# Kernel tuning notes

Measured on AMD Instinct MI355X. Metric: run time of the kernel, lower is better.

Reference implementation:

```python
import jax, jax.numpy as jnp
import numpy as np

NUM_CODES = 100000
NUM_EDGES = 20000
DIM = 128
DEG = 32  # nodes per hyperedge -> 640000 incidences


def setup_inputs() -> dict:
    key = jax.random.key(0)
    k1, k2, k3, k4, k5 = jax.random.split(key, 5)
    n_inc = NUM_EDGES * DEG
    # incidence list: edge_ids is sorted (CSR-style), node_ids are member nodes
    node_ids = jax.random.randint(k1, (n_inc,), 0, NUM_CODES, dtype=jnp.int32)
    edge_ids = jnp.repeat(jnp.arange(NUM_EDGES, dtype=jnp.int32), DEG)
    # learned parameters (xavier-ish scales)
    node_emb = jax.random.normal(k2, (NUM_CODES, DIM), jnp.float32) * (1.0 / np.sqrt(DIM))
    edge_emb = jax.random.normal(k3, (NUM_EDGES, DIM), jnp.float32) * (1.0 / np.sqrt(DIM))
    W_e = jax.random.normal(k4, (DIM, DIM), jnp.float32) * (1.0 / np.sqrt(DIM))
    b_e = jnp.zeros((DIM,), jnp.float32)
    W_v = jax.random.normal(k5, (DIM, DIM), jnp.float32) * (1.0 / np.sqrt(DIM))
    b_v = jnp.zeros((DIM,), jnp.float32)
    return {"node_emb": node_emb, "edge_emb": edge_emb, "W_e": W_e, "b_e": b_e,
            "W_v": W_v, "b_v": b_v, "node_ids": node_ids, "edge_ids": edge_ids}


def reference(node_emb, edge_emb, W_e, b_e, W_v, b_v, node_ids, edge_ids):
    N, D = node_emb.shape
    E = edge_emb.shape[0]
    # node -> edge: mean of member node embeddings per hyperedge (segment mean)
    gathered = node_emb[node_ids]                                    # [I, D]
    seg_sum = jax.ops.segment_sum(gathered, edge_ids, num_segments=E)  # [E, D]
    seg_cnt = jax.ops.segment_sum(jnp.ones_like(edge_ids, jnp.float32), edge_ids, num_segments=E)
    mean = seg_sum / jnp.maximum(seg_cnt, 1.0)[:, None]
    # empty edges fall back to their own edge embedding (as in the torch loop)
    edge_ctx = jnp.where(seg_cnt[:, None] > 0, mean, edge_emb)
    edge_ctx = edge_ctx @ W_e.T + b_e                                # lin_e
    # edge -> node: scatter-add edge_ctx back to member nodes
    node_sum = jnp.zeros_like(node_emb).at[node_ids].add(edge_ctx[edge_ids])
    deg = jnp.zeros((N,), jnp.float32).at[node_ids].add(1.0)
    node_cnt = 1.0 + deg  # torch code clamps zeros to 1 BEFORE adding counts
    node_ctx = (node_sum / node_cnt[:, None]) @ W_v.T + b_v          # lin_v
    node_out = node_emb + node_ctx
    edge_out = edge_emb + edge_ctx
    return (node_out, edge_out)
```

## Files before the change

### kernel.cpp

```cpp
#include <hip/hip_runtime.h>

#define DIMS 128
#define DEG 32
#define CAP 32

typedef __attribute__((ext_vector_type(8))) short short8;
typedef __attribute__((ext_vector_type(4))) float floatx4;

static __device__ __forceinline__ unsigned short f2bf(float f) {
  unsigned int u = __float_as_uint(f);
  unsigned int r = (u + 0x7FFFu + ((u >> 16) & 1u)) >> 16;
  return (unsigned short)r;
}
static __device__ __forceinline__ float bf2f(unsigned short v) {
  return __uint_as_float(((unsigned int)v) << 16);
}

__global__ __launch_bounds__(256) void k_prep(
    const float* __restrict__ node_emb, unsigned short* __restrict__ nb, int n0,
    const float* __restrict__ We_f, unsigned short* __restrict__ web, int n1,
    const float* __restrict__ Wv, const float* __restrict__ be,
    unsigned short* __restrict__ Wc, float* __restrict__ bc,
    int* __restrict__ cnt, int ncnt,
    unsigned short* __restrict__ zrow) {
  int b = blockIdx.x;
  int tid = threadIdx.x;
  if (b < 16) {
    __shared__ __align__(16) float wv_s[8][DIMS];
    int d0 = b * 8;
    {
      int row = tid >> 5, c4 = tid & 31;
      *(float4*)&wv_s[row][c4 * 4] = ((const float4*)(Wv + (size_t)d0 * DIMS))[tid];
    }
    __syncthreads();
    int dd = tid >> 5;
    int k4 = (tid & 31) * 4;
    float4 acc = {0.f, 0.f, 0.f, 0.f};
    for (int c = 0; c < DIMS; ++c) {
      float w = wv_s[dd][c];
      float4 we = *(const float4*)(We_f + (size_t)c * DIMS + k4);
      acc.x += w * we.x; acc.y += w * we.y; acc.z += w * we.z; acc.w += w * we.w;
    }
    ushort4 o;
    o.x = f2bf(acc.x); o.y = f2bf(acc.y); o.z = f2bf(acc.z); o.w = f2bf(acc.w);
    *(ushort4*)(Wc + (size_t)(d0 + dd) * DIMS + k4) = o;
    return;
  }
  if (b == 16) {
    __shared__ float be_s[DIMS];
    if (tid < DIMS) be_s[tid] = be[tid];
    if (tid >= 128 && tid < 144) {
      short8 z = {0, 0, 0, 0, 0, 0, 0, 0};
      *(short8*)(zrow + (size_t)(tid - 128) * 8) = z;
    }
    __syncthreads();
    if (tid < DIMS) {
      float s = 0.f;
      for (int c = 0; c < DIMS; ++c) s += Wv[(size_t)tid * DIMS + c] * be_s[c];
      bc[tid] = s;
    }
    return;
  }
  int base = (b - 17) * 256 + tid;
  int stride = (gridDim.x - 17) * 256;
  for (int t = base; t < ncnt; t += stride) cnt[t] = 0;
  int n4 = (n0 + n1) >> 2;
  for (int i4 = base; i4 < n4; i4 += stride) {
    int i = i4 * 4;
    const float* s; unsigned short* d;
    if (i < n0) { s = node_emb + i; d = nb + i; }
    else { s = We_f + (i - n0); d = web + (i - n0); }
    float4 v = *(const float4*)s;
    ushort4 o;
    o.x = f2bf(v.x); o.y = f2bf(v.y); o.z = f2bf(v.z); o.w = f2bf(v.w);
    *(ushort4*)d = o;
  }
}

__global__ __launch_bounds__(256) void k_edge_fused(
    const unsigned short* __restrict__ node_emb_bf,
    const int* __restrict__ node_ids,
    const unsigned short* __restrict__ We,
    const unsigned short* __restrict__ Wc,
    const float* __restrict__ be,
    const float* __restrict__ bc,
    const float* __restrict__ edge_emb,
    float* __restrict__ edge_out,
    unsigned short* __restrict__ ectx2,
    int* __restrict__ cnt,
    unsigned short* __restrict__ bucket,
    int E) {
  int e0 = blockIdx.x * 16;
  int tid = threadIdx.x;
  __shared__ int ids[16][DEG];
  __shared__ __align__(16) unsigned short xs[16 * DIMS];
#pragma unroll
  for (int u = 0; u < 2; ++u) {
    int idx = tid + u * 256;
    int ee = idx >> 5, j = idx & 31;
    int e = e0 + ee;
    ids[ee][j] = (e < E) ? node_ids[(size_t)e * DEG + j] : 0;
  }
  __syncthreads();

  {
    int ee = tid >> 4;
    int l8 = tid & 15;
    float acc[8] = {0.f, 0.f, 0.f, 0.f, 0.f, 0.f, 0.f, 0.f};
#pragma unroll
    for (int jb = 0; jb < DEG; jb += 8) {
      short8 v[8];
#pragma unroll
      for (int u = 0; u < 8; ++u) {
        int n = ids[ee][jb + u];
        v[u] = *(const short8*)(node_emb_bf + (size_t)n * DIMS + l8 * 8);
      }
#pragma unroll
      for (int u = 0; u < 8; ++u)
#pragma unroll
        for (int t = 0; t < 8; ++t) acc[t] += bf2f((unsigned short)v[u][t]);
    }
    const float s = 1.0f / (float)DEG;
    short8 o;
#pragma unroll
    for (int t = 0; t < 8; ++t) o[t] = (short)f2bf(acc[t] * s);
    int byt = ee * 256 + ((l8 * 16) ^ ((ee & 7) << 4));
    *(short8*)((char*)xs + byt) = o;
  }

  {
    int ia = tid, ib = tid + 256;
    int ea = e0 + (ia >> 5), eb = e0 + (ib >> 5);
    int na = ids[ia >> 5][ia & 31];
    int nb_ = ids[ib >> 5][ib & 31];
    int pa = CAP, pb = CAP;
    bool va = ea < E, vb = eb < E;
    if (va) pa = atomicAdd(&cnt[na], 1);
    if (vb) pb = atomicAdd(&cnt[nb_], 1);
    if (va && pa < CAP) bucket[(size_t)na * CAP + pa] = (unsigned short)ea;
    if (vb && pb < CAP) bucket[(size_t)nb_ * CAP + pb] = (unsigned short)eb;
  }
  __syncthreads();

  int wave = tid >> 6;
  int lane = tid & 63;
  int ln = lane & 15;
  int quad = lane >> 4;

  floatx4 acc_e0 = {0.f,0.f,0.f,0.f}, acc_e1 = {0.f,0.f,0.f,0.f};
  floatx4 acc_c0 = {0.f,0.f,0.f,0.f}, acc_c1 = {0.f,0.f,0.f,0.f};

#pragma unroll
  for (int kc = 0; kc < 4; ++kc) {
    int bofs = ln * 256 + ((kc * 64 + quad * 16) ^ ((ln & 7) << 4));
    short8 a = *(const short8*)((const char*)xs + bofs);
    int kb = kc * 32 + quad * 8;
    int wr0 = wave * 32 + ln;
    int wr1 = wave * 32 + 16 + ln;
    short8 bwe0 = *(const short8*)(We + (size_t)wr0 * DIMS + kb);
    short8 bwc0 = *(const short8*)(Wc + (size_t)wr0 * DIMS + kb);
    short8 bwe1 = *(const short8*)(We + (size_t)wr1 * DIMS + kb);
    short8 bwc1 = *(const short8*)(Wc + (size_t)wr1 * DIMS + kb);
    acc_e0 = __builtin_amdgcn_mfma_f32_16x16x32_bf16(bwe0, a, acc_e0, 0, 0, 0);
    acc_c0 = __builtin_amdgcn_mfma_f32_16x16x32_bf16(bwc0, a, acc_c0, 0, 0, 0);
    acc_e1 = __builtin_amdgcn_mfma_f32_16x16x32_bf16(bwe1, a, acc_e1, 0, 0, 0);
    acc_c1 = __builtin_amdgcn_mfma_f32_16x16x32_bf16(bwc1, a, acc_c1, 0, 0, 0);
  }

  int rE = e0 + ln;
  if (rE >= E) return;
#pragma unroll
  for (int t = 0; t < 2; ++t) {
    floatx4 ae = t ? acc_e1 : acc_e0;
    floatx4 ac = t ? acc_c1 : acc_c0;
    int c0 = wave * 32 + t * 16 + quad * 4;
    size_t off = (size_t)rE * DIMS + c0;
    float4 bev = *(const float4*)(be + c0);
    float4 rv = *(const float4*)(edge_emb + off);
    float4 ve;
    ve.x = ae[0] + bev.x + rv.x;
    ve.y = ae[1] + bev.y + rv.y;
    ve.z = ae[2] + bev.z + rv.z;
    ve.w = ae[3] + bev.w + rv.w;
    *(float4*)(edge_out + off) = ve;

    float4 bcv = *(const float4*)(bc + c0);
    ushort4 oc;
    oc.x = f2bf(ac[0] + bcv.x);
    oc.y = f2bf(ac[1] + bcv.y);
    oc.z = f2bf(ac[2] + bcv.z);
    oc.w = f2bf(ac[3] + bcv.w);
    *(ushort4*)(ectx2 + off) = oc;
  }
}

__global__ __launch_bounds__(256) void k_node_out(
    const unsigned short* __restrict__ ectx2,
    const unsigned short* __restrict__ bucket,
    const int* __restrict__ cnt,
    const unsigned short* __restrict__ node_emb_bf,
    const float* __restrict__ bv,
    float* __restrict__ node_out,
    int N, int E) {
  int n0 = blockIdx.x * 16;
  int tid = threadIdx.x;
  int nn = tid >> 4;
  int l8 = tid & 15;
  int n = n0 + nn;
  int nc = (n < N) ? n : (N - 1);
  short8 rb = *(const short8*)(node_emb_bf + (size_t)nc * DIMS + l8 * 8);
  float4 bv0 = *(const float4*)(bv + l8 * 8);
  float4 bv1 = *(const float4*)(bv + l8 * 8 + 4);

  __shared__ unsigned short elist[16][CAP];
  __shared__ float scale_s[16];
  __shared__ int cnt_s[16];
  {
    int p = tid & 15;
    unsigned int v = (n < N)
        ? ((const unsigned int*)(bucket + (size_t)n * CAP))[p] : 0u;
    elist[nn][p * 2] = (unsigned short)(v & 0xFFFFu);
    elist[nn][p * 2 + 1] = (unsigned short)(v >> 16);
  }
  if (tid < 16) {
    int nq = n0 + tid;
    int c = (nq < N) ? cnt[nq] : 0;
    scale_s[tid] = 1.0f / (1.0f + (float)c);
    cnt_s[tid] = c > CAP ? CAP : c;
  }
  __syncthreads();
  if (n >= N) return;
  int c = cnt_s[nn];
  float acc[8] = {0.f, 0.f, 0.f, 0.f, 0.f, 0.f, 0.f, 0.f};
  {
    short8 v[8];
#pragma unroll
    for (int u = 0; u < 8; ++u) {
      int idx = (u < c) ? (int)elist[nn][u] : E;
      v[u] = *(const short8*)(ectx2 + (size_t)idx * DIMS + l8 * 8);
    }
#pragma unroll
    for (int u = 0; u < 8; ++u)
#pragma unroll
      for (int t = 0; t < 8; ++t) acc[t] += bf2f((unsigned short)v[u][t]);
  }
  if (__any(c > 8)) {
    short8 v[8];
#pragma unroll
    for (int u = 0; u < 8; ++u) {
      int idx = (u + 8 < c) ? (int)elist[nn][u + 8] : E;
      v[u] = *(const short8*)(ectx2 + (size_t)idx * DIMS + l8 * 8);
    }
#pragma unroll
    for (int u = 0; u < 8; ++u)
#pragma unroll
      for (int t = 0; t < 8; ++t) acc[t] += bf2f((unsigned short)v[u][t]);
  }
  for (int j = 16; j < c; ++j) {
    short8 v = *(const short8*)(ectx2 + (size_t)elist[nn][j] * DIMS + l8 * 8);
#pragma unroll
    for (int t = 0; t < 8; ++t) acc[t] += bf2f((unsigned short)v[t]);
  }
  float sc = scale_s[nn];
  float4 o0, o1;
  o0.x = acc[0] * sc + bf2f((unsigned short)rb[0]) + bv0.x;
  o0.y = acc[1] * sc + bf2f((unsigned short)rb[1]) + bv0.y;
  o0.z = acc[2] * sc + bf2f((unsigned short)rb[2]) + bv0.z;
  o0.w = acc[3] * sc + bf2f((unsigned short)rb[3]) + bv0.w;
  o1.x = acc[4] * sc + bf2f((unsigned short)rb[4]) + bv1.x;
  o1.y = acc[5] * sc + bf2f((unsigned short)rb[5]) + bv1.y;
  o1.z = acc[6] * sc + bf2f((unsigned short)rb[6]) + bv1.z;
  o1.w = acc[7] * sc + bf2f((unsigned short)rb[7]) + bv1.w;
  float* dst = node_out + (size_t)n * DIMS + l8 * 8;
  *(float4*)dst = o0;
  *(float4*)(dst + 4) = o1;
}

extern "C" void kernel_launch(void* const* d_in, const int* in_sizes, int n_in,
                              void* d_out, int out_size, void* d_ws, size_t ws_size,
                              hipStream_t stream) {
  const float* node_emb = (const float*)d_in[0];
  const float* edge_emb = (const float*)d_in[1];
  const float* W_e      = (const float*)d_in[2];
  const float* b_e      = (const float*)d_in[3];
  const float* W_v      = (const float*)d_in[4];
  const float* b_v      = (const float*)d_in[5];
  const int*   node_ids = (const int*)d_in[6];

  const int N = in_sizes[0] / DIMS;
  const int E = in_sizes[1] / DIMS;

  float* out      = (float*)d_out;
  float* node_out = out;
  float* edge_out = out + (size_t)N * DIMS;

  unsigned short* nb    = (unsigned short*)d_ws;
  unsigned short* ectx2 = nb + (size_t)N * DIMS;
  unsigned short* web   = ectx2 + (size_t)(E + 1) * DIMS;
  unsigned short* wcb   = web + DIMS * DIMS;
  float* bc  = (float*)(wcb + DIMS * DIMS);
  int* cntb   = (int*)(bc + DIMS);
  unsigned short* bucket = (unsigned short*)(cntb + N);

  k_prep<<<17 + 2048, 256, 0, stream>>>(
      node_emb, nb, N * DIMS, W_e, web, DIMS * DIMS,
      W_v, b_e, wcb, bc, cntb, N, ectx2 + (size_t)E * DIMS);

  k_edge_fused<<<(E + 15) / 16, 256, 0, stream>>>(
      nb, node_ids, web, wcb, b_e, bc, edge_emb, edge_out, ectx2,
      cntb, bucket, E);

  k_node_out<<<(N + 15) / 16, 256, 0, stream>>>(
      ectx2, bucket, cntb, nb, b_v, node_out, N, E);
}
```

Baseline: 198.6 us.

## Stage W_e in LDS, reorder atomics before gather, unroll tail, nontemporal stores

Several unrelated tweaks land together. The prep kernel stages all of W_e in shared memory (64KB) before the weight-product loop instead of re-reading it from global memory. The edge kernel issues its bucket atomics before the node-embedding gather, so atomic latency can overlap with the gather loads. The node kernel replaces the masked second 8-wide batch with a 4-way unrolled loop over the remaining edges, and writes node_out with nontemporal stores. Risks are lower occupancy in the prep blocks from the large LDS footprint and less load batching for nodes with 9-15 edges.

```diff
diff --git a/kernel.cpp b/kernel.cpp
--- a/kernel.cpp
+++ b/kernel.cpp
@@ -26,8 +26,15 @@
   int b = blockIdx.x;
   int tid = threadIdx.x;
   if (b < 16) {
+    __shared__ __align__(16) float We_s[DIMS][DIMS];
     __shared__ __align__(16) float wv_s[8][DIMS];
     int d0 = b * 8;
+#pragma unroll
+    for (int u = 0; u < 16; ++u) {
+      int idx = tid + u * 256;
+      int row = idx >> 5, c4 = idx & 31;
+      *(float4*)&We_s[row][c4 * 4] = ((const float4*)We_f)[idx];
+    }
     {
       int row = tid >> 5, c4 = tid & 31;
       *(float4*)&wv_s[row][c4 * 4] = ((const float4*)(Wv + (size_t)d0 * DIMS))[tid];
@@ -38,7 +45,7 @@
     float4 acc = {0.f, 0.f, 0.f, 0.f};
     for (int c = 0; c < DIMS; ++c) {
       float w = wv_s[dd][c];
-      float4 we = *(const float4*)(We_f + (size_t)c * DIMS + k4);
+      float4 we = *(const float4*)&We_s[c][k4];
       acc.x += w * we.x; acc.y += w * we.y; acc.z += w * we.z; acc.w += w * we.w;
     }
     ushort4 o;
@@ -104,31 +111,6 @@
   __syncthreads();
 
   {
-    int ee = tid >> 4;
-    int l8 = tid & 15;
-    float acc[8] = {0.f, 0.f, 0.f, 0.f, 0.f, 0.f, 0.f, 0.f};
-#pragma unroll
-    for (int jb = 0; jb < DEG; jb += 8) {
-      short8 v[8];
-#pragma unroll
-      for (int u = 0; u < 8; ++u) {
-        int n = ids[ee][jb + u];
-        v[u] = *(const short8*)(node_emb_bf + (size_t)n * DIMS + l8 * 8);
-      }
-#pragma unroll
-      for (int u = 0; u < 8; ++u)
-#pragma unroll
-        for (int t = 0; t < 8; ++t) acc[t] += bf2f((unsigned short)v[u][t]);
-    }
-    const float s = 1.0f / (float)DEG;
-    short8 o;
-#pragma unroll
-    for (int t = 0; t < 8; ++t) o[t] = (short)f2bf(acc[t] * s);
-    int byt = ee * 256 + ((l8 * 16) ^ ((ee & 7) << 4));
-    *(short8*)((char*)xs + byt) = o;
-  }
-
-  {
     int ia = tid, ib = tid + 256;
     int ea = e0 + (ia >> 5), eb = e0 + (ib >> 5);
     int na = ids[ia >> 5][ia & 31];
@@ -139,6 +121,31 @@
     if (vb) pb = atomicAdd(&cnt[nb_], 1);
     if (va && pa < CAP) bucket[(size_t)na * CAP + pa] = (unsigned short)ea;
     if (vb && pb < CAP) bucket[(size_t)nb_ * CAP + pb] = (unsigned short)eb;
+  }
+
+  {
+    int ee = tid >> 4;
+    int l8 = tid & 15;
+    float acc[8] = {0.f, 0.f, 0.f, 0.f, 0.f, 0.f, 0.f, 0.f};
+#pragma unroll
+    for (int jb = 0; jb < DEG; jb += 8) {
+      short8 v[8];
+#pragma unroll
+      for (int u = 0; u < 8; ++u) {
+        int n = ids[ee][jb + u];
+        v[u] = *(const short8*)(node_emb_bf + (size_t)n * DIMS + l8 * 8);
+      }
+#pragma unroll
+      for (int u = 0; u < 8; ++u)
+#pragma unroll
+        for (int t = 0; t < 8; ++t) acc[t] += bf2f((unsigned short)v[u][t]);
+    }
+    const float s = 1.0f / (float)DEG;
+    short8 o;
+#pragma unroll
+    for (int t = 0; t < 8; ++t) o[t] = (short)f2bf(acc[t] * s);
+    int byt = ee * 256 + ((l8 * 16) ^ ((ee & 7) << 4));
+    *(short8*)((char*)xs + byt) = o;
   }
   __syncthreads();
 
@@ -244,36 +251,35 @@
 #pragma unroll
       for (int t = 0; t < 8; ++t) acc[t] += bf2f((unsigned short)v[u][t]);
   }
-  if (__any(c > 8)) {
-    short8 v[8];
-#pragma unroll
-    for (int u = 0; u < 8; ++u) {
-      int idx = (u + 8 < c) ? (int)elist[nn][u + 8] : E;
-      v[u] = *(const short8*)(ectx2 + (size_t)idx * DIMS + l8 * 8);
-    }
-#pragma unroll
-    for (int u = 0; u < 8; ++u)
-#pragma unroll
-      for (int t = 0; t < 8; ++t) acc[t] += bf2f((unsigned short)v[u][t]);
-  }
-  for (int j = 16; j < c; ++j) {
+  int j = 8;
+  for (; j + 4 <= c; j += 4) {
+    short8 v0 = *(const short8*)(ectx2 + (size_t)elist[nn][j + 0] * DIMS + l8 * 8);
+    short8 v1 = *(const short8*)(ectx2 + (size_t)elist[nn][j + 1] * DIMS + l8 * 8);
+    short8 v2 = *(const short8*)(ectx2 + (size_t)elist[nn][j + 2] * DIMS + l8 * 8);
+    short8 v3 = *(const short8*)(ectx2 + (size_t)elist[nn][j + 3] * DIMS + l8 * 8);
+#pragma unroll
+    for (int t = 0; t < 8; ++t)
+      acc[t] += bf2f((unsigned short)v0[t]) + bf2f((unsigned short)v1[t]) +
+                bf2f((unsigned short)v2[t]) + bf2f((unsigned short)v3[t]);
+  }
+  for (; j < c; ++j) {
     short8 v = *(const short8*)(ectx2 + (size_t)elist[nn][j] * DIMS + l8 * 8);
 #pragma unroll
     for (int t = 0; t < 8; ++t) acc[t] += bf2f((unsigned short)v[t]);
   }
   float sc = scale_s[nn];
-  float4 o0, o1;
-  o0.x = acc[0] * sc + bf2f((unsigned short)rb[0]) + bv0.x;
-  o0.y = acc[1] * sc + bf2f((unsigned short)rb[1]) + bv0.y;
-  o0.z = acc[2] * sc + bf2f((unsigned short)rb[2]) + bv0.z;
-  o0.w = acc[3] * sc + bf2f((unsigned short)rb[3]) + bv0.w;
-  o1.x = acc[4] * sc + bf2f((unsigned short)rb[4]) + bv1.x;
-  o1.y = acc[5] * sc + bf2f((unsigned short)rb[5]) + bv1.y;
-  o1.z = acc[6] * sc + bf2f((unsigned short)rb[6]) + bv1.z;
-  o1.w = acc[7] * sc + bf2f((unsigned short)rb[7]) + bv1.w;
+  floatx4 o0, o1;
+  o0[0] = acc[0] * sc + bf2f((unsigned short)rb[0]) + bv0.x;
+  o0[1] = acc[1] * sc + bf2f((unsigned short)rb[1]) + bv0.y;
+  o0[2] = acc[2] * sc + bf2f((unsigned short)rb[2]) + bv0.z;
+  o0[3] = acc[3] * sc + bf2f((unsigned short)rb[3]) + bv0.w;
+  o1[0] = acc[4] * sc + bf2f((unsigned short)rb[4]) + bv1.x;
+  o1[1] = acc[5] * sc + bf2f((unsigned short)rb[5]) + bv1.y;
+  o1[2] = acc[6] * sc + bf2f((unsigned short)rb[6]) + bv1.z;
+  o1[3] = acc[7] * sc + bf2f((unsigned short)rb[7]) + bv1.w;
   float* dst = node_out + (size_t)n * DIMS + l8 * 8;
-  *(float4*)dst = o0;
-  *(float4*)(dst + 4) = o1;
+  __builtin_nontemporal_store(o0, (floatx4*)dst);
+  __builtin_nontemporal_store(o1, (floatx4*)(dst + 4));
 }
 
 extern "C" void kernel_launch(void* const* d_in, const int* in_sizes, int n_in,
```

New measurement: 209.5 us. 1.05x slower.
